# Performance work log

Measured on AMD Instinct MI355X. Metric: run time of the kernel, lower is better.

Reference implementation:

```python
import jax, jax.numpy as jnp
import numpy as np

T, D, F, E, K = 8192, 1024, 512, 8, 2


def setup_inputs() -> dict:
    key = jax.random.key(0)
    k0, k1, k2, k3, k4 = jax.random.split(key, 5)
    hidden_states = jax.random.normal(k0, (T, D), dtype=jnp.float32)
    top_k_index = jax.random.randint(k1, (T, K), 0, E)
    top_k_weights = jax.random.uniform(k2, (T, K), dtype=jnp.float32)
    gate_up_proj = jax.random.normal(k3, (E, 2 * F, D), dtype=jnp.float32) * 0.02
    down_proj = jax.random.normal(k4, (E, D, F), dtype=jnp.float32) * 0.02
    return dict(hidden_states=hidden_states, top_k_index=top_k_index,
                top_k_weights=top_k_weights, gate_up_proj=gate_up_proj,
                down_proj=down_proj)


def reference(hidden_states, top_k_index, top_k_weights, gate_up_proj, down_proj):
    # hidden_states: [T, D]; top_k_index/weights: [T, K]
    # gate_up_proj: [E, 2F, D]; down_proj: [E, D, F]
    num_experts = gate_up_proj.shape[0]
    out = jnp.zeros_like(hidden_states)
    for e in range(num_experts):  # fixed small expert set
        # combined routing weight for expert e per token (sums duplicate k-slots,
        # matching index_add_ of per-slot contributions of identical expert output)
        w_e = jnp.sum(jnp.where(top_k_index == e, top_k_weights, 0.0), axis=-1)  # [T]
        gu = hidden_states @ gate_up_proj[e].T          # [T, 2F]
        gate, up = jnp.split(gu, 2, axis=-1)            # [T, F] each
        act = jax.nn.silu(gate) * up                    # SiLU-mul (LigerSiLUMulFunction)
        out = out + (act @ down_proj[e].T) * w_e[:, None]
    return out
```

## Files before the change

### kernel.cpp

```cpp
#include <hip/hip_runtime.h>
#include <cstdint>
#include <cstddef>

#define T_TOK 8192
#define DIM   1024
#define FF    512
#define NE    8
#define NSLOT 16384
#define BM    128
#define MAXBLK (NSLOT / BM + NE)

typedef short s16x8 __attribute__((ext_vector_type(8)));
typedef float f32x4 __attribute__((ext_vector_type(4)));

__device__ __forceinline__ unsigned int f2bf(float f) {
    union { float f; unsigned int u; } v; v.f = f;
    return (v.u + 0x7FFFu + ((v.u >> 16) & 1u)) >> 16;
}
__device__ __forceinline__ float bf2f(unsigned short b) {
    union { unsigned int u; float f; } v; v.u = ((unsigned int)b) << 16;
    return v.f;
}
__device__ __forceinline__ int pack2(float a, float b) {
    return (int)f2bf(a) | ((int)f2bf(b) << 16);
}
__device__ __forceinline__ int4 cvt8(const float* p) {
    float4 x = *(const float4*)p;
    float4 y = *(const float4*)(p + 4);
    int4 r;
    r.x = pack2(x.x, x.y); r.y = pack2(x.z, x.w);
    r.z = pack2(y.x, y.y); r.w = pack2(y.z, y.w);
    return r;
}

__device__ __forceinline__ void gload16(const unsigned short* g, unsigned short* l) {
    __builtin_amdgcn_global_load_lds(
        (const __attribute__((address_space(1))) void*)g,
        (__attribute__((address_space(3))) void*)l, 16, 0, 0);
}

__global__ __launch_bounds__(256) void route_count(const int* __restrict__ idx,
                                                   int* __restrict__ partial) {
    __shared__ int cnt[NE];
    const int tid = threadIdx.x;
    if (tid < NE) cnt[tid] = 0;
    __syncthreads();
    atomicAdd(&cnt[idx[blockIdx.x * 256 + tid]], 1);
    __syncthreads();
    if (tid < NE) partial[blockIdx.x * NE + tid] = cnt[tid];
}

__global__ void route_scan(const int* __restrict__ partial, int* offsets, int* cursor,
                           int* blk_e, int* blk_by) {
    __shared__ int counts_s[NE];
    const int tid = threadIdx.x;
    if (tid < NE) {
        int s = 0;
        for (int b = 0; b < 64; ++b) s += partial[b * NE + tid];
        counts_s[tid] = s;
    }
    __syncthreads();
    if (tid == 0) {
        int acc = 0, nb = 0;
        for (int e = 0; e < NE; ++e) {
            offsets[e] = acc; cursor[e] = acc;
            const int nby = (counts_s[e] + BM - 1) / BM;
            for (int b = 0; b < nby; ++b) { blk_e[nb] = e; blk_by[nb] = b; ++nb; }
            acc += counts_s[e];
        }
        offsets[NE] = acc;
        for (int b = nb; b < MAXBLK; ++b) { blk_e[b] = -1; blk_by[b] = 0; }
    }
}
__global__ void route_scatter(const int* __restrict__ idx, int* cursor,
                              int* row_slot, int* slot_pos) {
    int s = blockIdx.x * 256 + threadIdx.x;
    if (s < NSLOT) {
        int e = idx[s];
        int p = atomicAdd(&cursor[e], 1);
        row_slot[p] = s;
        slot_pos[s] = p;
    }
}

__global__ void cvt_all(const float* __restrict__ h, const float* __restrict__ g,
                        const float* __restrict__ d,
                        unsigned short* __restrict__ hb, unsigned short* __restrict__ gb,
                        unsigned short* __restrict__ db) {
    const int N1 = T_TOK * DIM / 8;
    const int N2 = NE * 2 * FF * DIM / 8;
    const int N3 = NE * DIM * FF / 8;
    const int stride = gridDim.x * 256;
    for (int i = blockIdx.x * 256 + threadIdx.x; i < N1 + N2 + N3; i += stride) {
        const float* s; unsigned short* o; int j;
        if (i < N1)            { s = h; o = hb; j = i; }
        else if (i < N1 + N2)  { s = g; o = gb; j = i - N1; }
        else                   { s = d; o = db; j = i - N1 - N2; }
        *(int4*)(o + (size_t)j * 8) = cvt8(s + (size_t)j * 8);
    }
}


#define G1_STAGE(BA, BB, T) do {                                                        \
    const int kn_ = (T) * 64;                                                           \
    _Pragma("unroll") for (int i_ = 0; i_ < 4; ++i_)                                    \
        gload16(hb + aoff[i_] + kn_, (BA) + (wv * 64 + i_ * 256) * 8);                  \
    _Pragma("unroll") for (int i_ = 0; i_ < 4; ++i_)                                    \
        gload16(gupb + boff[i_] + kn_, (BB) + (wv * 64 + i_ * 256) * 8);                \
} while (0)

#define G1_COMPUTE(BA, BB) do {                                                         \
    const char* Abc_ = (const char*)(BA);                                               \
    const char* Bbc_ = (const char*)(BB);                                               \
    _Pragma("unroll") for (int kk = 0; kk < 2; ++kk) {                                  \
        const int kc = kk * 4 + (lane >> 4);                                            \
        s16x8 af[4], bg[2], bu[2];                                                      \
        _Pragma("unroll") for (int m = 0; m < 4; ++m) {                                 \
            const int r = wr * 64 + m * 16 + (lane & 15);                               \
            af[m] = *(const s16x8*)(Abc_ + r * 128 + ((kc ^ (r & 7)) << 4)); }          \
        _Pragma("unroll") for (int n = 0; n < 2; ++n) {                                 \
            const int rg = wc * 32 + n * 16 + (lane & 15);                              \
            bg[n] = *(const s16x8*)(Bbc_ + rg * 128 + ((kc ^ (rg & 7)) << 4));          \
            const int ru = rg + 64;                                                     \
            bu[n] = *(const s16x8*)(Bbc_ + ru * 128 + ((kc ^ (ru & 7)) << 4)); }        \
        _Pragma("unroll") for (int m = 0; m < 4; ++m)                                   \
        _Pragma("unroll") for (int n = 0; n < 2; ++n) {                                 \
            ag[m][n] = __builtin_amdgcn_mfma_f32_16x16x32_bf16(af[m], bg[n], ag[m][n], 0, 0, 0); \
            au[m][n] = __builtin_amdgcn_mfma_f32_16x16x32_bf16(af[m], bu[n], au[m][n], 0, 0, 0); } \
    }                                                                                   \
} while (0)

__global__ __launch_bounds__(256) void gemm1_bf16(
    const unsigned short* __restrict__ hb,
    const unsigned short* __restrict__ gupb,
    const int* __restrict__ row_slot,
    const int* __restrict__ offsets,
    const int* __restrict__ blk_e,
    const int* __restrict__ blk_by,
    unsigned short* __restrict__ act)
{
    const int e = blk_e[blockIdx.y];
    if (e < 0) return;
    const int bx      = blockIdx.x;
    const int lby     = blk_by[blockIdx.y];
    const int rowbase = offsets[e] + lby * BM;
    const int rowlim  = offsets[e + 1] - 1;
    const int nrows   = min(BM, offsets[e + 1] - rowbase);

    __shared__ __align__(16) unsigned short Ab0[BM * 64], Ab1[BM * 64];
    __shared__ __align__(16) unsigned short Bb0[128 * 64], Bb1[128 * 64];

    const int tid  = threadIdx.x;
    const int lane = tid & 63;
    const int wv   = tid >> 6;
    const int wr   = wv >> 1, wc = wv & 1;

    int aoff[4];
#pragma unroll
    for (int i = 0; i < 4; ++i) {
        const int ch = tid + i * 256;
        const int r = ch >> 3, c = ch & 7;
        int grow = rowbase + r; if (grow > rowlim) grow = rowlim;
        const int tok = row_slot[grow] >> 1;
        aoff[i] = tok * DIM + ((c ^ (r & 7)) << 3);
    }
    int boff[4];
#pragma unroll
    for (int i = 0; i < 4; ++i) {
        const int ch = tid + i * 256;
        const int r = ch >> 3, c = ch & 7;
        const int gr = (r < 64) ? (bx * 64 + r) : (FF + bx * 64 + r - 64);
        boff[i] = e * (2 * FF * DIM) + gr * DIM + ((c ^ (r & 7)) << 3);
    }

    const f32x4 zf = {0.f, 0.f, 0.f, 0.f};
    f32x4 ag[4][2], au[4][2];
#pragma unroll
    for (int m = 0; m < 4; ++m)
#pragma unroll
        for (int n = 0; n < 2; ++n) { ag[m][n] = zf; au[m][n] = zf; }

    G1_STAGE(Ab0, Bb0, 0);
    __syncthreads();

#pragma unroll 1
    for (int t = 0; t < DIM / 64; t += 2) {
        G1_STAGE(Ab1, Bb1, t + 1);
        G1_COMPUTE(Ab0, Bb0);
        __syncthreads();
        if (t + 2 < DIM / 64) G1_STAGE(Ab0, Bb0, t + 2);
        G1_COMPUTE(Ab1, Bb1);
        __syncthreads();
    }

#pragma unroll
    for (int m = 0; m < 4; ++m)
#pragma unroll
        for (int n = 0; n < 2; ++n) {
            const int col = bx * 64 + wc * 32 + n * 16 + (lane & 15);
#pragma unroll
            for (int i = 0; i < 4; ++i) {
                const int rl = wr * 64 + m * 16 + ((lane >> 4) << 2) + i;
                if (rl < nrows) {
                    const float g = ag[m][n][i];
                    const float u = au[m][n][i];
                    const float a = (g / (1.f + __expf(-g))) * u;
                    act[(size_t)(rowbase + rl) * FF + col] = (unsigned short)f2bf(a);
                }
            }
        }
}

#define G2_STAGE(BA, BB, T) do {                                                        \
    const int kn_ = (T) * 64;                                                           \
    _Pragma("unroll") for (int i_ = 0; i_ < 4; ++i_)                                    \
        gload16(act + aoff[i_] + kn_, (BA) + (wv * 64 + i_ * 256) * 8);                 \
    _Pragma("unroll") for (int i_ = 0; i_ < 4; ++i_)                                    \
        gload16(downb + boff[i_] + kn_, (BB) + (wv * 64 + i_ * 256) * 8);               \
} while (0)

#define G2_COMPUTE(BA, BB) do {                                                         \
    const char* Abc_ = (const char*)(BA);                                               \
    const char* Bbc_ = (const char*)(BB);                                               \
    _Pragma("unroll") for (int kk = 0; kk < 2; ++kk) {                                  \
        const int kc = kk * 4 + (lane >> 4);                                            \
        s16x8 af[4], bf[4];                                                             \
        _Pragma("unroll") for (int m = 0; m < 4; ++m) {                                 \
            const int r = wr * 64 + m * 16 + (lane & 15);                               \
            af[m] = *(const s16x8*)(Abc_ + r * 128 + ((kc ^ (r & 7)) << 4)); }          \
        _Pragma("unroll") for (int n = 0; n < 4; ++n) {                                 \
            const int r = wc * 64 + n * 16 + (lane & 15);                               \
            bf[n] = *(const s16x8*)(Bbc_ + r * 128 + ((kc ^ (r & 7)) << 4)); }          \
        _Pragma("unroll") for (int m = 0; m < 4; ++m)                                   \
        _Pragma("unroll") for (int n = 0; n < 4; ++n)                                   \
            acc[m][n] = __builtin_amdgcn_mfma_f32_16x16x32_bf16(af[m], bf[n], acc[m][n], 0, 0, 0); \
    }                                                                                   \
} while (0)

template <int MODE>
__global__ __launch_bounds__(256) void gemm2_slot(
    const unsigned short* __restrict__ act,
    const unsigned short* __restrict__ downb,
    const int* __restrict__ row_slot,
    const int* __restrict__ offsets,
    const int* __restrict__ blk_e,
    const int* __restrict__ blk_by,
    void* __restrict__ outslot)
{
    const int e = blk_e[blockIdx.y];
    if (e < 0) return;
    const int bx      = blockIdx.x;
    const int lby     = blk_by[blockIdx.y];
    const int rowbase = offsets[e] + lby * BM;
    const int nrows   = min(BM, offsets[e + 1] - rowbase);
    const int rowlim  = offsets[e + 1] - 1;

    __shared__ __align__(16) unsigned short Ab0[BM * 64], Ab1[BM * 64];
    __shared__ __align__(16) unsigned short Bb0[128 * 64], Bb1[128 * 64];

    const int tid  = threadIdx.x;
    const int lane = tid & 63;
    const int wv   = tid >> 6;
    const int wr   = wv >> 1, wc = wv & 1;

    int aoff[4];
#pragma unroll
    for (int i = 0; i < 4; ++i) {
        const int ch = tid + i * 256;
        const int r = ch >> 3, c = ch & 7;
        int grow = rowbase + r; if (grow > rowlim) grow = rowlim;
        aoff[i] = grow * FF + ((c ^ (r & 7)) << 3);
    }
    int boff[4];
#pragma unroll
    for (int i = 0; i < 4; ++i) {
        const int ch = tid + i * 256;
        const int r = ch >> 3, c = ch & 7;
        boff[i] = e * (DIM * FF) + (bx * 128 + r) * FF + ((c ^ (r & 7)) << 3);
    }

    const f32x4 zf = {0.f, 0.f, 0.f, 0.f};
    f32x4 acc[4][4];
#pragma unroll
    for (int m = 0; m < 4; ++m)
#pragma unroll
        for (int n = 0; n < 4; ++n) acc[m][n] = zf;

    G2_STAGE(Ab0, Bb0, 0);
    __syncthreads();

#pragma unroll 1
    for (int t = 0; t < FF / 64; t += 2) {
        G2_STAGE(Ab1, Bb1, t + 1);
        G2_COMPUTE(Ab0, Bb0);
        __syncthreads();
        if (t + 2 < FF / 64) G2_STAGE(Ab0, Bb0, t + 2);
        G2_COMPUTE(Ab1, Bb1);
        __syncthreads();
    }

#pragma unroll
    for (int m = 0; m < 4; ++m)
#pragma unroll
        for (int i = 0; i < 4; ++i) {
            const int rl = wr * 64 + m * 16 + ((lane >> 4) << 2) + i;
            if (rl < nrows) {
                const size_t base = (size_t)(rowbase + rl) * DIM + bx * 128 + wc * 64 + (lane & 15);
                if (MODE == 1) {
                    float* o = (float*)outslot + base;
#pragma unroll
                    for (int n = 0; n < 4; ++n) o[n * 16] = acc[m][n][i];
                } else {
                    unsigned short* o = (unsigned short*)outslot + base;
#pragma unroll
                    for (int n = 0; n < 4; ++n) o[n * 16] = (unsigned short)f2bf(acc[m][n][i]);
                }
            }
        }
}

template <int MODE>
__global__ __launch_bounds__(256) void combine_k(
    const void* __restrict__ outslot,
    const int* __restrict__ slot_pos,
    const float* __restrict__ tkw,
    float* __restrict__ out)
{
    const int i = blockIdx.x * 256 + threadIdx.x;
    const int t = i >> 7;
    const int d = (i & 127) << 3;
    const int p0 = slot_pos[2 * t], p1 = slot_pos[2 * t + 1];
    const float w0 = tkw[2 * t],    w1 = tkw[2 * t + 1];
    float r0[8], r1[8];
    if (MODE == 1) {
        const float* s0 = (const float*)outslot + (size_t)p0 * DIM + d;
        const float* s1 = (const float*)outslot + (size_t)p1 * DIM + d;
        float4 a0 = *(const float4*)s0, a1 = *(const float4*)(s0 + 4);
        float4 b0 = *(const float4*)s1, b1 = *(const float4*)(s1 + 4);
        r0[0]=a0.x; r0[1]=a0.y; r0[2]=a0.z; r0[3]=a0.w; r0[4]=a1.x; r0[5]=a1.y; r0[6]=a1.z; r0[7]=a1.w;
        r1[0]=b0.x; r1[1]=b0.y; r1[2]=b0.z; r1[3]=b0.w; r1[4]=b1.x; r1[5]=b1.y; r1[6]=b1.z; r1[7]=b1.w;
    } else {
        const s16x8 a = *(const s16x8*)((const unsigned short*)outslot + (size_t)p0 * DIM + d);
        const s16x8 b = *(const s16x8*)((const unsigned short*)outslot + (size_t)p1 * DIM + d);
#pragma unroll
        for (int j = 0; j < 8; ++j) { r0[j] = bf2f((unsigned short)a[j]); r1[j] = bf2f((unsigned short)b[j]); }
    }
    float4 o0, o1;
    o0.x = w0*r0[0]+w1*r1[0]; o0.y = w0*r0[1]+w1*r1[1]; o0.z = w0*r0[2]+w1*r1[2]; o0.w = w0*r0[3]+w1*r1[3];
    o1.x = w0*r0[4]+w1*r1[4]; o1.y = w0*r0[5]+w1*r1[5]; o1.z = w0*r0[6]+w1*r1[6]; o1.w = w0*r0[7]+w1*r1[7];
    float* op = out + (size_t)t * DIM + d;
    *(float4*)op = o0;
    *(float4*)(op + 4) = o1;
}


__global__ __launch_bounds__(256) void moe_gemm1(
    const float* __restrict__ hidden, const float* __restrict__ gup,
    const int* __restrict__ row_slot, const int* __restrict__ offsets,
    unsigned short* __restrict__ act)
{
    const int e = blockIdx.z;
    const int row0 = offsets[e];
    const int n_e = offsets[e + 1] - row0;
    const int by = blockIdx.y;
    if (by * 128 >= n_e) return;
    const int bx = blockIdx.x;
    __shared__ __align__(16) unsigned short Abuf[128 * 64];
    __shared__ __align__(16) unsigned short Bbuf[128 * 64];
    char* Ab = (char*)Abuf; char* Bb = (char*)Bbuf;
    const int tid = threadIdx.x, lane = tid & 63, wv = tid >> 6;
    const int wr = wv >> 1, wc = wv & 1;
    const float* aptr[4]; const float* bptr[4]; int soff[4];
#pragma unroll
    for (int i = 0; i < 4; ++i) {
        const int chunk = tid + i * 256;
        const int r = chunk >> 3, c = chunk & 7;
        soff[i] = r * 128 + ((c ^ (r & 7)) << 4);
        int rr = by * 128 + r; if (rr >= n_e) rr = n_e - 1;
        const int slot = row_slot[row0 + rr];
        aptr[i] = hidden + (size_t)(slot >> 1) * DIM + c * 8;
        const int gr = (r < 64) ? (bx * 64 + r) : (FF + bx * 64 + (r - 64));
        bptr[i] = gup + (size_t)e * (2 * FF * DIM) + (size_t)gr * DIM + c * 8;
    }
    const f32x4 zf = {0.f, 0.f, 0.f, 0.f};
    f32x4 acc_g[4][2], acc_u[4][2];
#pragma unroll
    for (int m = 0; m < 4; ++m)
#pragma unroll
        for (int n = 0; n < 2; ++n) { acc_g[m][n] = zf; acc_u[m][n] = zf; }
    for (int k0 = 0; k0 < DIM; k0 += 64) {
        __syncthreads();
#pragma unroll
        for (int i = 0; i < 4; ++i) *(int4*)(Ab + soff[i]) = cvt8(aptr[i] + k0);
#pragma unroll
        for (int i = 0; i < 4; ++i) *(int4*)(Bb + soff[i]) = cvt8(bptr[i] + k0);
        __syncthreads();
#pragma unroll
        for (int kk = 0; kk < 2; ++kk) {
            const int kc = kk * 4 + (lane >> 4);
            s16x8 af[4], bg[2], bu[2];
#pragma unroll
            for (int m = 0; m < 4; ++m) {
                const int r = wr * 64 + m * 16 + (lane & 15);
                af[m] = *(const s16x8*)(Ab + r * 128 + ((kc ^ (r & 7)) << 4));
            }
#pragma unroll
            for (int n = 0; n < 2; ++n) {
                const int rg = wc * 32 + n * 16 + (lane & 15);
                bg[n] = *(const s16x8*)(Bb + rg * 128 + ((kc ^ (rg & 7)) << 4));
                const int ru = rg + 64;
                bu[n] = *(const s16x8*)(Bb + ru * 128 + ((kc ^ (ru & 7)) << 4));
            }
#pragma unroll
            for (int m = 0; m < 4; ++m)
#pragma unroll
                for (int n = 0; n < 2; ++n) {
                    acc_g[m][n] = __builtin_amdgcn_mfma_f32_16x16x32_bf16(af[m], bg[n], acc_g[m][n], 0, 0, 0);
                    acc_u[m][n] = __builtin_amdgcn_mfma_f32_16x16x32_bf16(af[m], bu[n], acc_u[m][n], 0, 0, 0);
                }
        }
    }
#pragma unroll
    for (int m = 0; m < 4; ++m)
#pragma unroll
        for (int n = 0; n < 2; ++n) {
            const int col = bx * 64 + wc * 32 + n * 16 + (lane & 15);
#pragma unroll
            for (int i = 0; i < 4; ++i) {
                const int rl = wr * 64 + m * 16 + ((lane >> 4) << 2) + i;
                const int rr = by * 128 + rl;
                if (rr < n_e) {
                    const float g = acc_g[m][n][i];
                    const float u = acc_u[m][n][i];
                    const float a = (g / (1.f + __expf(-g))) * u;
                    act[(size_t)(row0 + rr) * FF + col] = (unsigned short)f2bf(a);
                }
            }
        }
}

__global__ __launch_bounds__(256) void moe_gemm2(
    const unsigned short* __restrict__ act, const float* __restrict__ down,
    const int* __restrict__ row_slot, const int* __restrict__ offsets,
    const float* __restrict__ tkw, float* __restrict__ out)
{
    const int e = blockIdx.z;
    const int row0 = offsets[e];
    const int n_e = offsets[e + 1] - row0;
    const int by = blockIdx.y;
    if (by * 128 >= n_e) return;
    const int bx = blockIdx.x;
    __shared__ __align__(16) unsigned short Abuf[128 * 64];
    __shared__ __align__(16) unsigned short Bbuf[128 * 64];
    char* Ab = (char*)Abuf; char* Bb = (char*)Bbuf;
    const int tid = threadIdx.x, lane = tid & 63, wv = tid >> 6;
    const int wr = wv >> 1, wc = wv & 1;
    const unsigned short* aptr[4]; const float* bptr[4]; int soff[4];
#pragma unroll
    for (int i = 0; i < 4; ++i) {
        const int chunk = tid + i * 256;
        const int r = chunk >> 3, c = chunk & 7;
        soff[i] = r * 128 + ((c ^ (r & 7)) << 4);
        int rr = by * 128 + r; if (rr >= n_e) rr = n_e - 1;
        aptr[i] = act + (size_t)(row0 + rr) * FF + c * 8;
        bptr[i] = down + (size_t)e * (DIM * FF) + (size_t)(bx * 128 + r) * FF + c * 8;
    }
    const f32x4 zf = {0.f, 0.f, 0.f, 0.f};
    f32x4 acc[4][4];
#pragma unroll
    for (int m = 0; m < 4; ++m)
#pragma unroll
        for (int n = 0; n < 4; ++n) acc[m][n] = zf;
    for (int k0 = 0; k0 < FF; k0 += 64) {
        __syncthreads();
#pragma unroll
        for (int i = 0; i < 4; ++i) *(int4*)(Ab + soff[i]) = *(const int4*)(aptr[i] + k0);
#pragma unroll
        for (int i = 0; i < 4; ++i) *(int4*)(Bb + soff[i]) = cvt8(bptr[i] + k0);
        __syncthreads();
#pragma unroll
        for (int kk = 0; kk < 2; ++kk) {
            const int kc = kk * 4 + (lane >> 4);
            s16x8 af[4], bf[4];
#pragma unroll
            for (int m = 0; m < 4; ++m) {
                const int r = wr * 64 + m * 16 + (lane & 15);
                af[m] = *(const s16x8*)(Ab + r * 128 + ((kc ^ (r & 7)) << 4));
            }
#pragma unroll
            for (int n = 0; n < 4; ++n) {
                const int r = wc * 64 + n * 16 + (lane & 15);
                bf[n] = *(const s16x8*)(Bb + r * 128 + ((kc ^ (r & 7)) << 4));
            }
#pragma unroll
            for (int m = 0; m < 4; ++m)
#pragma unroll
                for (int n = 0; n < 4; ++n)
                    acc[m][n] = __builtin_amdgcn_mfma_f32_16x16x32_bf16(af[m], bf[n], acc[m][n], 0, 0, 0);
        }
    }
#pragma unroll
    for (int m = 0; m < 4; ++m)
#pragma unroll
        for (int i = 0; i < 4; ++i) {
            const int rl = wr * 64 + m * 16 + ((lane >> 4) << 2) + i;
            const int rr = by * 128 + rl;
            if (rr < n_e) {
                const int slot = row_slot[row0 + rr];
                const float w = tkw[slot];
                float* orow = out + (size_t)(slot >> 1) * DIM + bx * 128 + wc * 64 + (lane & 15);
#pragma unroll
                for (int n = 0; n < 4; ++n)
                    unsafeAtomicAdd(orow + n * 16, acc[m][n][i] * w);
            }
        }
}

extern "C" void kernel_launch(void* const* d_in, const int* in_sizes, int n_in,
                              void* d_out, int out_size, void* d_ws, size_t ws_size,
                              hipStream_t stream)
{
    const float* hidden = (const float*)d_in[0];
    const int*   idx    = (const int*)  d_in[1];
    const float* tkw    = (const float*)d_in[2];
    const float* gup    = (const float*)d_in[3];
    const float* down   = (const float*)d_in[4];
    float* out = (float*)d_out;

    const size_t ACT = (size_t)NSLOT * FF * 2;
    const size_t HB  = (size_t)T_TOK * DIM * 2;
    const size_t GB  = (size_t)NE * 2 * FF * DIM * 2;
    const size_t DB  = (size_t)NE * DIM * FF * 2;
    const size_t RS  = (size_t)NSLOT * 4;
    const size_t SP  = (size_t)NSLOT * 4;
    const size_t CTRL = 8192;
    const size_t OS32 = (size_t)NSLOT * DIM * 4;
    const size_t OS16 = (size_t)NSLOT * DIM * 2;
    char* ws = (char*)d_ws;
    unsigned short* act = (unsigned short*)ws;

    const size_t base_need = ACT + HB + GB + DB + RS + SP + CTRL;
    int mode;
    if      (ws_size >= base_need + OS32) mode = 1;
    else if (ws_size >= base_need + OS16) mode = 2;
    else if (ws_size >= ACT + RS + SP + CTRL) mode = 0;
    else mode = -1;
    if (mode < 0) return;

    unsigned short *hb = nullptr, *gb = nullptr, *db = nullptr;
    int *row_slot, *ctrl; void* outslot = nullptr;
    if (mode == 1 || mode == 2) {
        hb = (unsigned short*)(ws + ACT);
        gb = (unsigned short*)(ws + ACT + HB);
        db = (unsigned short*)(ws + ACT + HB + GB);
        row_slot = (int*)(ws + ACT + HB + GB + DB);
        ctrl     = (int*)(ws + ACT + HB + GB + DB + RS + SP);
        outslot  = (void*)(ws + base_need);
    } else {
        row_slot = (int*)(ws + ACT);
        ctrl     = (int*)(ws + ACT + RS + SP);
    }
    int* slot_pos = row_slot + NSLOT;
    int* offsets = ctrl;
    int* blk_e   = ctrl + 16;
    int* blk_by  = ctrl + 16 + MAXBLK;
    int* cursor  = ctrl + 16 + 2 * MAXBLK;
    int* partial = cursor + 8;

    if (mode == 0)
        hipMemsetAsync(out, 0, (size_t)T_TOK * DIM * sizeof(float), stream);

    route_count  <<<NSLOT / 256, 256, 0, stream>>>(idx, partial);
    route_scan   <<<1, 64, 0, stream>>>(partial, offsets, cursor, blk_e, blk_by);
    route_scatter<<<NSLOT / 256, 256, 0, stream>>>(idx, cursor, row_slot, slot_pos);

    if (mode == 1 || mode == 2) {
        cvt_all<<<2048, 256, 0, stream>>>(hidden, gup, down, hb, gb, db);
        gemm1_bf16<<<dim3(FF / 64, MAXBLK), 256, 0, stream>>>(
            hb, gb, row_slot, offsets, blk_e, blk_by, act);
        if (mode == 1) {
            gemm2_slot<1><<<dim3(DIM / 128, MAXBLK), 256, 0, stream>>>(
                act, db, row_slot, offsets, blk_e, blk_by, outslot);
            combine_k<1><<<T_TOK * DIM / 8 / 256, 256, 0, stream>>>(outslot, slot_pos, tkw, out);
        } else {
            gemm2_slot<2><<<dim3(DIM / 128, MAXBLK), 256, 0, stream>>>(
                act, db, row_slot, offsets, blk_e, blk_by, outslot);
            combine_k<2><<<T_TOK * DIM / 8 / 256, 256, 0, stream>>>(outslot, slot_pos, tkw, out);
        }
    } else {
        moe_gemm1<<<dim3(FF / 64, 128, NE), 256, 0, stream>>>(hidden, gup, row_slot, offsets, act);
        moe_gemm2<<<dim3(DIM / 128, 128, NE), 256, 0, stream>>>(act, down, row_slot, offsets, tkw, out);
    }
}
```

Before: 211.1 us.

## Enlarge first expert GEMM tile to 256x128 with 512-thread blocks

The gate/up GEMM now uses 256-row token blocks and 128 gate plus 128 up columns per block, with 8 waves, and route_scan builds a second block map for the larger row tiles. Larger tiles raise arithmetic intensity and cut redundant global loads of hidden rows and weights. In exchange it uses more LDS (128KB double-buffered) and more accumulator registers, and fewer, larger blocks mean more padding waste per expert and possibly lower occupancy or tail imbalance.

After: 213.8 us. Within noise of the previous version (+1.3%).

```diff
diff --git a/kernel.cpp b/kernel.cpp
--- a/kernel.cpp
+++ b/kernel.cpp
@@ -9,6 +9,8 @@
 #define NSLOT 16384
 #define BM    128
 #define MAXBLK (NSLOT / BM + NE)
+#define BM1   256
+#define MAXB1 (NSLOT / BM1 + NE)
 
 typedef short s16x8 __attribute__((ext_vector_type(8)));
 typedef float f32x4 __attribute__((ext_vector_type(4)));
@@ -51,7 +53,7 @@
 }
 
 __global__ void route_scan(const int* __restrict__ partial, int* offsets, int* cursor,
-                           int* blk_e, int* blk_by) {
+                           int* blk_e, int* blk_by, int* blk_e1, int* blk_by1) {
     __shared__ int counts_s[NE];
     const int tid = threadIdx.x;
     if (tid < NE) {
@@ -61,15 +63,18 @@
     }
     __syncthreads();
     if (tid == 0) {
-        int acc = 0, nb = 0;
+        int acc = 0, nb = 0, nb1 = 0;
         for (int e = 0; e < NE; ++e) {
             offsets[e] = acc; cursor[e] = acc;
             const int nby = (counts_s[e] + BM - 1) / BM;
             for (int b = 0; b < nby; ++b) { blk_e[nb] = e; blk_by[nb] = b; ++nb; }
+            const int nby1 = (counts_s[e] + BM1 - 1) / BM1;
+            for (int b = 0; b < nby1; ++b) { blk_e1[nb1] = e; blk_by1[nb1] = b; ++nb1; }
             acc += counts_s[e];
         }
         offsets[NE] = acc;
         for (int b = nb; b < MAXBLK; ++b) { blk_e[b] = -1; blk_by[b] = 0; }
+        for (int b = nb1; b < MAXB1; ++b) { blk_e1[b] = -1; blk_by1[b] = 0; }
     }
 }
 __global__ void route_scatter(const int* __restrict__ idx, int* cursor,
@@ -104,9 +109,9 @@
 #define G1_STAGE(BA, BB, T) do {                                                        \
     const int kn_ = (T) * 64;                                                           \
     _Pragma("unroll") for (int i_ = 0; i_ < 4; ++i_)                                    \
-        gload16(hb + aoff[i_] + kn_, (BA) + (wv * 64 + i_ * 256) * 8);                  \
+        gload16(hb + aoff[i_] + kn_, (BA) + (wv * 64 + i_ * 512) * 8);                  \
     _Pragma("unroll") for (int i_ = 0; i_ < 4; ++i_)                                    \
-        gload16(gupb + boff[i_] + kn_, (BB) + (wv * 64 + i_ * 256) * 8);                \
+        gload16(gupb + boff[i_] + kn_, (BB) + (wv * 64 + i_ * 512) * 8);                \
 } while (0)
 
 #define G1_COMPUTE(BA, BB) do {                                                         \
@@ -114,69 +119,63 @@
     const char* Bbc_ = (const char*)(BB);                                               \
     _Pragma("unroll") for (int kk = 0; kk < 2; ++kk) {                                  \
         const int kc = kk * 4 + (lane >> 4);                                            \
-        s16x8 af[4], bg[2], bu[2];                                                      \
-        _Pragma("unroll") for (int m = 0; m < 4; ++m) {                                 \
-            const int r = wr * 64 + m * 16 + (lane & 15);                               \
+        s16x8 af[8], bg[2], bu[2];                                                      \
+        _Pragma("unroll") for (int m = 0; m < 8; ++m) {                                 \
+            const int r = wr * 128 + m * 16 + (lane & 15);                              \
             af[m] = *(const s16x8*)(Abc_ + r * 128 + ((kc ^ (r & 7)) << 4)); }          \
         _Pragma("unroll") for (int n = 0; n < 2; ++n) {                                 \
-            const int rg = wc * 32 + n * 16 + (lane & 15);                              \
+            const int rg = wn * 32 + n * 16 + (lane & 15);                              \
             bg[n] = *(const s16x8*)(Bbc_ + rg * 128 + ((kc ^ (rg & 7)) << 4));          \
-            const int ru = rg + 64;                                                     \
+            const int ru = rg + 128;                                                    \
             bu[n] = *(const s16x8*)(Bbc_ + ru * 128 + ((kc ^ (ru & 7)) << 4)); }        \
-        _Pragma("unroll") for (int m = 0; m < 4; ++m)                                   \
+        _Pragma("unroll") for (int m = 0; m < 8; ++m)                                   \
         _Pragma("unroll") for (int n = 0; n < 2; ++n) {                                 \
             ag[m][n] = __builtin_amdgcn_mfma_f32_16x16x32_bf16(af[m], bg[n], ag[m][n], 0, 0, 0); \
             au[m][n] = __builtin_amdgcn_mfma_f32_16x16x32_bf16(af[m], bu[n], au[m][n], 0, 0, 0); } \
     }                                                                                   \
 } while (0)
 
-__global__ __launch_bounds__(256) void gemm1_bf16(
+__global__ __launch_bounds__(512, 2) void gemm1_256(
     const unsigned short* __restrict__ hb,
     const unsigned short* __restrict__ gupb,
     const int* __restrict__ row_slot,
     const int* __restrict__ offsets,
-    const int* __restrict__ blk_e,
-    const int* __restrict__ blk_by,
+    const int* __restrict__ blk_e1,
+    const int* __restrict__ blk_by1,
     unsigned short* __restrict__ act)
 {
-    const int e = blk_e[blockIdx.y];
+    const int e = blk_e1[blockIdx.y];
     if (e < 0) return;
     const int bx      = blockIdx.x;
-    const int lby     = blk_by[blockIdx.y];
-    const int rowbase = offsets[e] + lby * BM;
+    const int rowbase = offsets[e] + blk_by1[blockIdx.y] * BM1;
     const int rowlim  = offsets[e + 1] - 1;
-    const int nrows   = min(BM, offsets[e + 1] - rowbase);
-
-    __shared__ __align__(16) unsigned short Ab0[BM * 64], Ab1[BM * 64];
-    __shared__ __align__(16) unsigned short Bb0[128 * 64], Bb1[128 * 64];
+    const int nrows   = min(BM1, offsets[e + 1] - rowbase);
+
+    __shared__ __align__(16) unsigned short Ab0[BM1 * 64], Ab1[BM1 * 64];
+    __shared__ __align__(16) unsigned short Bb0[256 * 64], Bb1[256 * 64];
 
     const int tid  = threadIdx.x;
     const int lane = tid & 63;
     const int wv   = tid >> 6;
-    const int wr   = wv >> 1, wc = wv & 1;
-
-    int aoff[4];
+    const int wr   = wv >> 2;
+    const int wn   = wv & 3;
+
+    int aoff[4], boff[4];
 #pragma unroll
     for (int i = 0; i < 4; ++i) {
-        const int ch = tid + i * 256;
+        const int ch = tid + i * 512;
         const int r = ch >> 3, c = ch & 7;
         int grow = rowbase + r; if (grow > rowlim) grow = rowlim;
         const int tok = row_slot[grow] >> 1;
         aoff[i] = tok * DIM + ((c ^ (r & 7)) << 3);
-    }
-    int boff[4];
-#pragma unroll
-    for (int i = 0; i < 4; ++i) {
-        const int ch = tid + i * 256;
-        const int r = ch >> 3, c = ch & 7;
-        const int gr = (r < 64) ? (bx * 64 + r) : (FF + bx * 64 + r - 64);
+        const int gr = (r < 128) ? (bx * 128 + r) : (FF + bx * 128 + r - 128);
         boff[i] = e * (2 * FF * DIM) + gr * DIM + ((c ^ (r & 7)) << 3);
     }
 
     const f32x4 zf = {0.f, 0.f, 0.f, 0.f};
-    f32x4 ag[4][2], au[4][2];
-#pragma unroll
-    for (int m = 0; m < 4; ++m)
+    f32x4 ag[8][2], au[8][2];
+#pragma unroll
+    for (int m = 0; m < 8; ++m)
 #pragma unroll
         for (int n = 0; n < 2; ++n) { ag[m][n] = zf; au[m][n] = zf; }
 
@@ -194,13 +193,13 @@
     }
 
 #pragma unroll
-    for (int m = 0; m < 4; ++m)
+    for (int m = 0; m < 8; ++m)
 #pragma unroll
         for (int n = 0; n < 2; ++n) {
-            const int col = bx * 64 + wc * 32 + n * 16 + (lane & 15);
+            const int col = bx * 128 + wn * 32 + n * 16 + (lane & 15);
 #pragma unroll
             for (int i = 0; i < 4; ++i) {
-                const int rl = wr * 64 + m * 16 + ((lane >> 4) << 2) + i;
+                const int rl = wr * 128 + m * 16 + ((lane >> 4) << 2) + i;
                 if (rl < nrows) {
                     const float g = ag[m][n][i];
                     const float u = au[m][n][i];
@@ -210,6 +209,7 @@
             }
         }
 }
+
 
 #define G2_STAGE(BA, BB, T) do {                                                        \
     const int kn_ = (T) * 64;                                                           \
@@ -564,20 +564,22 @@
     int* offsets = ctrl;
     int* blk_e   = ctrl + 16;
     int* blk_by  = ctrl + 16 + MAXBLK;
-    int* cursor  = ctrl + 16 + 2 * MAXBLK;
+    int* blk_e1  = ctrl + 16 + 2 * MAXBLK;
+    int* blk_by1 = ctrl + 16 + 2 * MAXBLK + MAXB1;
+    int* cursor  = ctrl + 16 + 2 * MAXBLK + 2 * MAXB1;
     int* partial = cursor + 8;
 
     if (mode == 0)
         hipMemsetAsync(out, 0, (size_t)T_TOK * DIM * sizeof(float), stream);
 
     route_count  <<<NSLOT / 256, 256, 0, stream>>>(idx, partial);
-    route_scan   <<<1, 64, 0, stream>>>(partial, offsets, cursor, blk_e, blk_by);
+    route_scan   <<<1, 64, 0, stream>>>(partial, offsets, cursor, blk_e, blk_by, blk_e1, blk_by1);
     route_scatter<<<NSLOT / 256, 256, 0, stream>>>(idx, cursor, row_slot, slot_pos);
 
     if (mode == 1 || mode == 2) {
         cvt_all<<<2048, 256, 0, stream>>>(hidden, gup, down, hb, gb, db);
-        gemm1_bf16<<<dim3(FF / 64, MAXBLK), 256, 0, stream>>>(
-            hb, gb, row_slot, offsets, blk_e, blk_by, act);
+        gemm1_256<<<dim3(FF / 128, MAXB1), 512, 0, stream>>>(
+            hb, gb, row_slot, offsets, blk_e1, blk_by1, act);
         if (mode == 1) {
             gemm2_slot<1><<<dim3(DIM / 128, MAXBLK), 256, 0, stream>>>(
                 act, db, row_slot, offsets, blk_e, blk_by, outslot);
```
